# Kernel tuning notes

Hardware: AMD Instinct MI355X
Metric: run time of the kernel (lower is better)

## Reference

```python
import jax, jax.numpy as jnp
import numpy as np

N, F_T, F_P = 10000, 128, 64
MAIN_CH, SEC_CH = 7, 32


def _glorot(key, shape):
    fan_in, fan_out = shape[0], shape[1]
    lim = np.sqrt(6.0 / (fan_in + fan_out))
    return jax.random.uniform(key, shape, jnp.float32, -lim, lim)


def setup_inputs() -> dict:
    key = jax.random.key(0)
    ks = jax.random.split(key, 16)
    return {
        "temporal_features": jax.random.normal(ks[0], (N, F_T), jnp.float32),
        "A": jax.random.uniform(ks[1], (N, N), jnp.float32) / 100.0,
        "path_features": jax.random.normal(ks[2], (N, F_P), jnp.float32),
        # secondary ARMAConv: in F_T -> SEC_CH
        "Ws1": _glorot(ks[3], (F_T, SEC_CH)),
        "Ws2": _glorot(ks[4], (F_T, SEC_CH)),
        "bs": jnp.zeros((SEC_CH,), jnp.float32),
        # main2 ARMAConv: in SEC_CH+F_P -> MAIN_CH
        "Wm2a": _glorot(ks[5], (SEC_CH + F_P, MAIN_CH)),
        "Wm2b": _glorot(ks[6], (SEC_CH + F_P, MAIN_CH)),
        "bm2": jnp.zeros((MAIN_CH,), jnp.float32),
        # main ARMAConv: in F_T+F_P -> MAIN_CH
        "Wma": _glorot(ks[7], (F_T + F_P, MAIN_CH)),
        "Wmb": _glorot(ks[8], (F_T + F_P, MAIN_CH)),
        "bm": jnp.zeros((MAIN_CH,), jnp.float32),
        # scalar combine weights (v_bias_out init 1.0, v_bias_out2 init 0.0;
        # use small random values so both branches carry gradient)
        "v1": jax.random.normal(ks[9], (), jnp.float32) + 1.0,
        "v2": jax.random.normal(ks[10], (), jnp.float32),
    }


def _arma_gcs(x, A, W1, W2, b):
    # one ARMA graph-conv step (iterations=1, order=1, dropout off at eval):
    # A @ (x W1) + x W2 + b
    return A @ (x @ W1) + x @ W2 + b


def reference(temporal_features, A, path_features,
              Ws1, Ws2, bs, Wm2a, Wm2b, bm2, Wma, Wmb, bm, v1, v2):
    # secondary conv: gcn_activation=relu, activation=relu -> relu once
    sec = jax.nn.relu(_arma_gcs(temporal_features, A, Ws1, Ws2, bs))
    sec = jnp.concatenate([sec, path_features], axis=-1)          # [N, SEC+F_P]
    main_sec = _arma_gcs(sec, A, Wm2a, Wm2b, bm2)                 # [N, MAIN_CH]
    main_in = jnp.concatenate([temporal_features, path_features], axis=-1)
    main = _arma_gcs(main_in, A, Wma, Wmb, bm)                    # [N, MAIN_CH]
    # stack([v2*main, v1*main_sec], -1).mean(-1) then softmax
    combined = 0.5 * (v2 * main + v1 * main_sec)
    return jax.nn.softmax(combined, axis=-1)
```

## Files before the change

### kernel.cpp

```cpp
#include <hip/hip_runtime.h>
#include <math.h>

#define N_NODES 10000
#define FT 128
#define FP 64
#define SEC 32
#define MC 7
#define C1 39
#define KTILE 64
#define RB 64
#define NTILES 157
#define KZ 4

__global__ __launch_bounds__(256) void k1_lin(
    const float* __restrict__ T, const float* __restrict__ P,
    const float* __restrict__ Ws1, const float* __restrict__ Ws2,
    const float* __restrict__ bs, const float* __restrict__ Wma,
    const float* __restrict__ Wmb, const float* __restrict__ bm,
    float* __restrict__ P1, float* __restrict__ Z2, float* __restrict__ Zm) {
  __shared__ float Tl[8 * FT];
  __shared__ float Pl[8 * FP];
  int t = threadIdx.x;
  int r0 = blockIdx.x * 8;
  #pragma unroll
  for (int j = 0; j < 4; ++j) {
    int f = t + 256 * j;
    int r = f >> 7, k = f & 127;
    int row = r0 + r;
    Tl[f] = (row < N_NODES) ? T[row * FT + k] : 0.f;
  }
  #pragma unroll
  for (int j = 0; j < 2; ++j) {
    int f = t + 256 * j;
    int r = f >> 6, k = f & 63;
    int row = r0 + r;
    Pl[f] = (row < N_NODES) ? P[row * FP + k] : 0.f;
  }
  __syncthreads();
  int r = t >> 5, c = t & 31;
  int row = r0 + r;
  const float* trow = &Tl[r * FT];
  const float* prow = &Pl[r * FP];
  float y1 = 0.f, z2 = 0.f;
  for (int k = 0; k < FT; ++k) {
    float tv = trow[k];
    y1 += tv * Ws1[k * SEC + c];
    z2 += tv * Ws2[k * SEC + c];
  }
  z2 += bs[c];
  if (row < N_NODES) {
    P1[row * C1 + c] = y1;
    Z2[row * SEC + c] = z2;
  }
  if (c < MC) {
    float ym = 0.f, zm = 0.f;
    for (int k = 0; k < FT; ++k) {
      float tv = trow[k];
      ym += tv * Wma[k * MC + c];
      zm += tv * Wmb[k * MC + c];
    }
    for (int u = 0; u < FP; ++u) {
      float pv = prow[u];
      ym += pv * Wma[(FT + u) * MC + c];
      zm += pv * Wmb[(FT + u) * MC + c];
    }
    zm += bm[c];
    if (row < N_NODES) {
      P1[row * C1 + SEC + c] = ym;
      Zm[row * MC + c] = zm;
    }
  }
}

__global__ __launch_bounds__(256) void k2_spmm(
    const float* __restrict__ A, const float* __restrict__ P1,
    float* __restrict__ Spart) {
  __shared__ float Al[5248];
  __shared__ float Yl[KTILE * 40];
  int t = threadIdx.x;
  int r0 = blockIdx.x * RB;
  int kz = blockIdx.y;
  int w = t >> 6, r = t & 63;
  float acc[C1];
  #pragma unroll
  for (int c = 0; c < C1; ++c) acc[c] = 0.f;

  for (int tile = kz; tile < NTILES; tile += KZ) {
    int kt = tile * KTILE;
    __syncthreads();
    #pragma unroll
    for (int j = 0; j < 4; ++j) {
      int f = t + 256 * j;
      int rr = f >> 4, c4 = (f & 15) * 4;
      int row = r0 + rr, k = kt + c4;
      float4 v = make_float4(0.f, 0.f, 0.f, 0.f);
      if (row < N_NODES && k < N_NODES)
        v = *(const float4*)&A[(size_t)row * N_NODES + k];
      float* d = &Al[rr * 65 + c4];
      d[0] = v.x; d[1] = v.y; d[2] = v.z; d[3] = v.w;
    }
    #pragma unroll
    for (int j = 0; j < 10; ++j) {
      int s = t + 256 * j;
      int kk = s / 40, cc = s - kk * 40;
      int kr = kt + kk;
      float v = 0.f;
      if (cc < C1 && kr < N_NODES) v = P1[kr * C1 + cc];
      Yl[s] = v;
    }
    __syncthreads();
    for (int j = 0; j < 16; ++j) {
      int kk = 4 * j + w;
      float a = Al[r * 65 + kk];
      const float* yrow = &Yl[kk * 40];
      #pragma unroll
      for (int c = 0; c < C1; ++c) acc[c] += a * yrow[c];
    }
  }
  __syncthreads();
  if (w & 1) {
    float* dst = &Al[(w >> 1) * 2624 + r * 41];
    #pragma unroll
    for (int c = 0; c < C1; ++c) dst[c] = acc[c];
  }
  __syncthreads();
  if (!(w & 1)) {
    const float* src = &Al[(w >> 1) * 2624 + r * 41];
    #pragma unroll
    for (int c = 0; c < C1; ++c) acc[c] += src[c];
  }
  __syncthreads();
  if (w == 2) {
    float* dst = &Al[r * 41];
    #pragma unroll
    for (int c = 0; c < C1; ++c) dst[c] = acc[c];
  }
  __syncthreads();
  if (w == 0) {
    const float* src = &Al[r * 41];
    #pragma unroll
    for (int c = 0; c < C1; ++c) acc[c] += src[c];
    int row = r0 + r;
    if (row < N_NODES) {
      float* dst = &Spart[((size_t)kz * N_NODES + row) * C1];
      #pragma unroll
      for (int c = 0; c < C1; ++c) dst[c] = acc[c];
    }
  }
}

__global__ __launch_bounds__(256) void k2b(
    const float* __restrict__ Spart, const float* __restrict__ Z2,
    const float* __restrict__ Zm, const float* __restrict__ v2p,
    float* __restrict__ sec, float* __restrict__ M0) {
  int g = blockIdx.x * 256 + threadIdx.x;
  if (g >= N_NODES * C1) return;
  int row = g / C1, c = g - row * C1;
  const size_t stride = (size_t)N_NODES * C1;
  float s = Spart[g] + Spart[stride + g] + Spart[2 * stride + g] + Spart[3 * stride + g];
  if (c < SEC) {
    s += Z2[row * SEC + c];
    sec[row * SEC + c] = fmaxf(s, 0.f);
  } else {
    int j = c - SEC;
    s += Zm[row * MC + j];
    M0[row * MC + j] = 0.5f * v2p[0] * s;
  }
}

__global__ __launch_bounds__(256) void k2c(
    const float* __restrict__ sec, const float* __restrict__ P,
    const float* __restrict__ Wm2a, const float* __restrict__ Wm2b,
    const float* __restrict__ bm2, const float* __restrict__ v1p,
    const float* __restrict__ M0, float* __restrict__ Y2, float* __restrict__ C0) {
  int g = blockIdx.x * 256 + threadIdx.x;
  if (g >= N_NODES * MC) return;
  int row = g / MC, j = g - row * MC;
  float y = 0.f, z = 0.f;
  for (int c = 0; c < SEC; ++c) {
    float sv = sec[row * SEC + c];
    y += sv * Wm2a[c * MC + j];
    z += sv * Wm2b[c * MC + j];
  }
  for (int u = 0; u < FP; ++u) {
    float pv = P[row * FP + u];
    y += pv * Wm2a[(SEC + u) * MC + j];
    z += pv * Wm2b[(SEC + u) * MC + j];
  }
  z += bm2[j];
  Y2[g] = y;
  C0[g] = M0[g] + 0.5f * v1p[0] * z;
}

__global__ __launch_bounds__(256) void k3_spmm(
    const float* __restrict__ A, const float* __restrict__ Y2,
    float* __restrict__ S2part) {
  __shared__ float Al[4160];
  __shared__ float Yl[KTILE * 8];
  int t = threadIdx.x;
  int r0 = blockIdx.x * RB;
  int kz = blockIdx.y;
  int w = t >> 6, r = t & 63;
  float acc[MC];
  #pragma unroll
  for (int c = 0; c < MC; ++c) acc[c] = 0.f;

  for (int tile = kz; tile < NTILES; tile += KZ) {
    int kt = tile * KTILE;
    __syncthreads();
    #pragma unroll
    for (int j = 0; j < 4; ++j) {
      int f = t + 256 * j;
      int rr = f >> 4, c4 = (f & 15) * 4;
      int row = r0 + rr, k = kt + c4;
      float4 v = make_float4(0.f, 0.f, 0.f, 0.f);
      if (row < N_NODES && k < N_NODES)
        v = *(const float4*)&A[(size_t)row * N_NODES + k];
      float* d = &Al[rr * 65 + c4];
      d[0] = v.x; d[1] = v.y; d[2] = v.z; d[3] = v.w;
    }
    #pragma unroll
    for (int j = 0; j < 2; ++j) {
      int s = t + 256 * j;
      int kk = s >> 3, cc = s & 7;
      int kr = kt + kk;
      float v = 0.f;
      if (cc < MC && kr < N_NODES) v = Y2[kr * MC + cc];
      Yl[s] = v;
    }
    __syncthreads();
    for (int j = 0; j < 16; ++j) {
      int kk = 4 * j + w;
      float a = Al[r * 65 + kk];
      const float* yrow = &Yl[kk * 8];
      #pragma unroll
      for (int c = 0; c < MC; ++c) acc[c] += a * yrow[c];
    }
  }
  __syncthreads();
  if (w & 1) {
    float* dst = &Al[(w >> 1) * 512 + r * 8];
    #pragma unroll
    for (int c = 0; c < MC; ++c) dst[c] = acc[c];
  }
  __syncthreads();
  if (!(w & 1)) {
    const float* src = &Al[(w >> 1) * 512 + r * 8];
    #pragma unroll
    for (int c = 0; c < MC; ++c) acc[c] += src[c];
  }
  __syncthreads();
  if (w == 2) {
    float* dst = &Al[r * 8];
    #pragma unroll
    for (int c = 0; c < MC; ++c) dst[c] = acc[c];
  }
  __syncthreads();
  if (w == 0) {
    const float* src = &Al[r * 8];
    #pragma unroll
    for (int c = 0; c < MC; ++c) acc[c] += src[c];
    int row = r0 + r;
    if (row < N_NODES) {
      float* dst = &S2part[((size_t)kz * N_NODES + row) * MC];
      #pragma unroll
      for (int c = 0; c < MC; ++c) dst[c] = acc[c];
    }
  }
}

__global__ __launch_bounds__(256) void k3b(
    const float* __restrict__ S2part, const float* __restrict__ C0,
    const float* __restrict__ v1p, float* __restrict__ out) {
  int row = blockIdx.x * 256 + threadIdx.x;
  if (row >= N_NODES) return;
  float v1h = 0.5f * v1p[0];
  const size_t stride = (size_t)N_NODES * MC;
  float comb[MC];
  float mx = -1e30f;
  #pragma unroll
  for (int j = 0; j < MC; ++j) {
    int g = row * MC + j;
    float s = S2part[g] + S2part[stride + g] + S2part[2 * stride + g] + S2part[3 * stride + g];
    float cv = C0[g] + v1h * s;
    comb[j] = cv;
    mx = fmaxf(mx, cv);
  }
  float sum = 0.f;
  #pragma unroll
  for (int j = 0; j < MC; ++j) {
    comb[j] = expf(comb[j] - mx);
    sum += comb[j];
  }
  float inv = 1.f / sum;
  #pragma unroll
  for (int j = 0; j < MC; ++j) out[row * MC + j] = comb[j] * inv;
}

extern "C" void kernel_launch(void* const* d_in, const int* in_sizes, int n_in,
                              void* d_out, int out_size, void* d_ws, size_t ws_size,
                              hipStream_t stream) {
  const float* T    = (const float*)d_in[0];
  const float* A    = (const float*)d_in[1];
  const float* P    = (const float*)d_in[2];
  const float* Ws1  = (const float*)d_in[3];
  const float* Ws2  = (const float*)d_in[4];
  const float* bs   = (const float*)d_in[5];
  const float* Wm2a = (const float*)d_in[6];
  const float* Wm2b = (const float*)d_in[7];
  const float* bm2  = (const float*)d_in[8];
  const float* Wma  = (const float*)d_in[9];
  const float* Wmb  = (const float*)d_in[10];
  const float* bm   = (const float*)d_in[11];
  const float* v1   = (const float*)d_in[12];
  const float* v2   = (const float*)d_in[13];
  float* out = (float*)d_out;

  float* ws = (float*)d_ws;
  float* P1     = ws;
  float* Z2     = P1 + (size_t)N_NODES * C1;
  float* Zm     = Z2 + (size_t)N_NODES * SEC;
  float* Spart  = Zm + (size_t)N_NODES * MC;
  float* sec    = Spart + (size_t)4 * N_NODES * C1;
  float* M0     = sec + (size_t)N_NODES * SEC;
  float* Y2     = M0 + (size_t)N_NODES * MC;
  float* C0     = Y2 + (size_t)N_NODES * MC;
  float* S2part = C0 + (size_t)N_NODES * MC;

  hipLaunchKernelGGL(k1_lin, dim3((N_NODES + 7) / 8), dim3(256), 0, stream,
                     T, P, Ws1, Ws2, bs, Wma, Wmb, bm, P1, Z2, Zm);
  hipLaunchKernelGGL(k2_spmm, dim3(NTILES, KZ), dim3(256), 0, stream, A, P1, Spart);
  hipLaunchKernelGGL(k2b, dim3((N_NODES * C1 + 255) / 256), dim3(256), 0, stream,
                     Spart, Z2, Zm, v2, sec, M0);
  hipLaunchKernelGGL(k2c, dim3((N_NODES * MC + 255) / 256), dim3(256), 0, stream,
                     sec, P, Wm2a, Wm2b, bm2, v1, M0, Y2, C0);
  hipLaunchKernelGGL(k3_spmm, dim3(NTILES, KZ), dim3(256), 0, stream, A, Y2, S2part);
  hipLaunchKernelGGL(k3b, dim3((N_NODES + 255) / 256), dim3(256), 0, stream,
                     S2part, C0, v1, out);
}
```

Baseline: 944.3 us.

## Use split-bf16 MFMA for dense A products with atomic split-K reduction

Both dense A-matmuls now run on MFMA 16x16x32 bf16 instructions. A and the feature matrices are split into hi/lo bf16 pairs and multiplied as three products to keep near-fp32 accuracy. Partial sums across eight K-splits are combined with atomicAdd into a zeroed buffer, replacing the four-way partial buffers and their reduction pass. The linear kernels are restructured to process 16 rows per block and write transposed bf16 features. The kernels remain bound by streaming the 400MB A twice, and the atomics and bf16 splitting add overhead and rounding risk.

```diff
diff --git a/kernel.cpp b/kernel.cpp
--- a/kernel.cpp
+++ b/kernel.cpp
@@ -1,170 +1,188 @@
 #include <hip/hip_runtime.h>
+#include <stdint.h>
 #include <math.h>
 
 #define N_NODES 10000
-#define FT 128
-#define FP 64
-#define SEC 32
-#define MC 7
-#define C1 39
-#define KTILE 64
-#define RB 64
+#define NPAD 10048
+#define KZ 8
 #define NTILES 157
-#define KZ 4
-
-__global__ __launch_bounds__(256) void k1_lin(
+
+using short8 = __attribute__((ext_vector_type(8))) short;
+using f32x4  = __attribute__((ext_vector_type(4))) float;
+
+__device__ __forceinline__ uint32_t fbits(float x){ union{float f;uint32_t u;} v; v.f=x; return v.u; }
+__device__ __forceinline__ float    fval(uint32_t u){ union{float f;uint32_t u;} v; v.u=u; return v.f; }
+
+__device__ __forceinline__ void split1(float a, uint16_t& h, uint16_t& l){
+  uint32_t ua = fbits(a);
+  float lo = a - fval(ua & 0xFFFF0000u);
+  h = (uint16_t)(ua >> 16);
+  l = (uint16_t)(fbits(lo) >> 16);
+}
+
+__device__ __forceinline__ void split2pack(float x, float y, uint32_t& hp, uint32_t& lp){
+  uint32_t ux = fbits(x), uy = fbits(y);
+  float lx = x - fval(ux & 0xFFFF0000u);
+  float ly = y - fval(uy & 0xFFFF0000u);
+  hp = (uy & 0xFFFF0000u) | (ux >> 16);
+  lp = (fbits(ly) & 0xFFFF0000u) | (fbits(lx) >> 16);
+}
+
+__global__ __launch_bounds__(256) void k1(
     const float* __restrict__ T, const float* __restrict__ P,
     const float* __restrict__ Ws1, const float* __restrict__ Ws2,
     const float* __restrict__ bs, const float* __restrict__ Wma,
     const float* __restrict__ Wmb, const float* __restrict__ bm,
-    float* __restrict__ P1, float* __restrict__ Z2, float* __restrict__ Zm) {
-  __shared__ float Tl[8 * FT];
-  __shared__ float Pl[8 * FP];
+    uint16_t* __restrict__ Yth, uint16_t* __restrict__ Ytl,
+    float* __restrict__ Z2, float* __restrict__ Zm) {
+  __shared__ float Xl[16 * 192];
+  __shared__ float RedY[16 * 7], RedZ[16 * 7];
   int t = threadIdx.x;
-  int r0 = blockIdx.x * 8;
-  #pragma unroll
-  for (int j = 0; j < 4; ++j) {
-    int f = t + 256 * j;
-    int r = f >> 7, k = f & 127;
+  int r0 = blockIdx.x * 16;
+  for (int s = t; s < 768; s += 256) {
+    int r = s / 48, c4 = (s % 48) * 4;
+    const float* src = (c4 < 128) ? &T[(size_t)(r0 + r) * 128 + c4]
+                                  : &P[(size_t)(r0 + r) * 64 + (c4 - 128)];
+    *(float4*)&Xl[r * 192 + c4] = *(const float4*)src;
+  }
+  __syncthreads();
+  {
+    int c = t & 31, r = t >> 5;
+    float y0 = 0, z0 = 0, y1 = 0, z1 = 0;
+    const float* x0 = &Xl[r * 192];
+    const float* x1 = &Xl[(r + 8) * 192];
+    #pragma unroll 8
+    for (int k = 0; k < 128; ++k) {
+      float w1 = Ws1[k * 32 + c], w2 = Ws2[k * 32 + c];
+      float a0 = x0[k], a1 = x1[k];
+      y0 += a0 * w1; z0 += a0 * w2;
+      y1 += a1 * w1; z1 += a1 * w2;
+    }
+    int rowA = r0 + r, rowB = r0 + r + 8;
+    float bsv = bs[c];
+    Z2[rowA * 32 + c] = z0 + bsv;
+    Z2[rowB * 32 + c] = z1 + bsv;
+    uint16_t h, l;
+    split1(y0, h, l); Yth[c * NPAD + rowA] = h; Ytl[c * NPAD + rowA] = l;
+    split1(y1, h, l); Yth[c * NPAD + rowB] = h; Ytl[c * NPAD + rowB] = l;
+  }
+  int u = t & 15, r = t >> 4;
+  int j = u % 7, half = u / 7;
+  float ym = 0, zm = 0;
+  if (u < 14) {
+    int kb = half * 96;
+    const float* xr = &Xl[r * 192];
+    #pragma unroll 4
+    for (int i = 0; i < 96; ++i) {
+      int k = kb + i;
+      float wa = Wma[k * 7 + j], wb = Wmb[k * 7 + j];
+      float xv = xr[k];
+      ym += xv * wa; zm += xv * wb;
+    }
+    if (half == 1) { RedY[r * 7 + j] = ym; RedZ[r * 7 + j] = zm; }
+  }
+  __syncthreads();
+  if (u < 7) {
+    ym += RedY[r * 7 + j]; zm += RedZ[r * 7 + j];
     int row = r0 + r;
-    Tl[f] = (row < N_NODES) ? T[row * FT + k] : 0.f;
-  }
-  #pragma unroll
-  for (int j = 0; j < 2; ++j) {
-    int f = t + 256 * j;
-    int r = f >> 6, k = f & 63;
-    int row = r0 + r;
-    Pl[f] = (row < N_NODES) ? P[row * FP + k] : 0.f;
-  }
-  __syncthreads();
-  int r = t >> 5, c = t & 31;
-  int row = r0 + r;
-  const float* trow = &Tl[r * FT];
-  const float* prow = &Pl[r * FP];
-  float y1 = 0.f, z2 = 0.f;
-  for (int k = 0; k < FT; ++k) {
-    float tv = trow[k];
-    y1 += tv * Ws1[k * SEC + c];
-    z2 += tv * Ws2[k * SEC + c];
-  }
-  z2 += bs[c];
-  if (row < N_NODES) {
-    P1[row * C1 + c] = y1;
-    Z2[row * SEC + c] = z2;
-  }
-  if (c < MC) {
-    float ym = 0.f, zm = 0.f;
-    for (int k = 0; k < FT; ++k) {
-      float tv = trow[k];
-      ym += tv * Wma[k * MC + c];
-      zm += tv * Wmb[k * MC + c];
-    }
-    for (int u = 0; u < FP; ++u) {
-      float pv = prow[u];
-      ym += pv * Wma[(FT + u) * MC + c];
-      zm += pv * Wmb[(FT + u) * MC + c];
-    }
-    zm += bm[c];
-    if (row < N_NODES) {
-      P1[row * C1 + SEC + c] = ym;
-      Zm[row * MC + c] = zm;
-    }
-  }
-}
-
-__global__ __launch_bounds__(256) void k2_spmm(
-    const float* __restrict__ A, const float* __restrict__ P1,
-    float* __restrict__ Spart) {
-  __shared__ float Al[5248];
-  __shared__ float Yl[KTILE * 40];
+    uint16_t h, l;
+    split1(ym, h, l);
+    Yth[(32 + j) * NPAD + row] = h; Ytl[(32 + j) * NPAD + row] = l;
+    Zm[row * 7 + j] = zm + bm[j];
+  }
+}
+
+template<int NCF, int NC, int CST>
+__global__ __launch_bounds__(256) void k_spmm(
+    const float* __restrict__ A, const uint16_t* __restrict__ Yth,
+    const uint16_t* __restrict__ Ytl, float* __restrict__ Sacc) {
+  __shared__ uint16_t Ah[64 * 72];
+  __shared__ uint16_t Al[64 * 72];
+  __shared__ uint16_t Yh[NCF * 16 * 72];
+  __shared__ uint16_t Yl[NCF * 16 * 72];
   int t = threadIdx.x;
-  int r0 = blockIdx.x * RB;
+  int r0 = blockIdx.x * 64;
   int kz = blockIdx.y;
-  int w = t >> 6, r = t & 63;
-  float acc[C1];
-  #pragma unroll
-  for (int c = 0; c < C1; ++c) acc[c] = 0.f;
+  int w = t >> 6, lane = t & 63;
+  int m = lane & 15, q = lane >> 4;
+  f32x4 acc[NCF];
+  #pragma unroll
+  for (int f = 0; f < NCF; ++f) acc[f] = (f32x4){0.f, 0.f, 0.f, 0.f};
 
   for (int tile = kz; tile < NTILES; tile += KZ) {
-    int kt = tile * KTILE;
+    int kt = tile * 64;
     __syncthreads();
     #pragma unroll
-    for (int j = 0; j < 4; ++j) {
-      int f = t + 256 * j;
-      int rr = f >> 4, c4 = (f & 15) * 4;
+    for (int jj = 0; jj < 4; ++jj) {
+      int fi = t + 256 * jj;
+      int rr = fi >> 4, c4 = (fi & 15) * 4;
       int row = r0 + rr, k = kt + c4;
       float4 v = make_float4(0.f, 0.f, 0.f, 0.f);
       if (row < N_NODES && k < N_NODES)
         v = *(const float4*)&A[(size_t)row * N_NODES + k];
-      float* d = &Al[rr * 65 + c4];
-      d[0] = v.x; d[1] = v.y; d[2] = v.z; d[3] = v.w;
-    }
+      uint32_t h0, l0, h1, l1;
+      split2pack(v.x, v.y, h0, l0);
+      split2pack(v.z, v.w, h1, l1);
+      uint2 hh; hh.x = h0; hh.y = h1;
+      uint2 ll; ll.x = l0; ll.y = l1;
+      *(uint2*)&Ah[rr * 72 + c4] = hh;
+      *(uint2*)&Al[rr * 72 + c4] = ll;
+    }
+    for (int s = t; s < NCF * 16 * 32; s += 256) {
+      int c = s >> 5, kk = s & 31;
+      int k2i = kt + 2 * kk;
+      uint32_t vh = 0, vl = 0;
+      if (c < NC && k2i < N_NODES) {
+        vh = *(const uint32_t*)&Yth[(size_t)c * NPAD + k2i];
+        vl = *(const uint32_t*)&Ytl[(size_t)c * NPAD + k2i];
+      }
+      *(uint32_t*)&Yh[c * 72 + 2 * kk] = vh;
+      *(uint32_t*)&Yl[c * 72 + 2 * kk] = vl;
+    }
+    __syncthreads();
     #pragma unroll
-    for (int j = 0; j < 10; ++j) {
-      int s = t + 256 * j;
-      int kk = s / 40, cc = s - kk * 40;
-      int kr = kt + kk;
-      float v = 0.f;
-      if (cc < C1 && kr < N_NODES) v = P1[kr * C1 + cc];
-      Yl[s] = v;
-    }
-    __syncthreads();
-    for (int j = 0; j < 16; ++j) {
-      int kk = 4 * j + w;
-      float a = Al[r * 65 + kk];
-      const float* yrow = &Yl[kk * 40];
+    for (int ks = 0; ks < 2; ++ks) {
+      int ko = ks * 32 + q * 8;
+      short8 ah = *(const short8*)&Ah[(16 * w + m) * 72 + ko];
+      short8 al = *(const short8*)&Al[(16 * w + m) * 72 + ko];
       #pragma unroll
-      for (int c = 0; c < C1; ++c) acc[c] += a * yrow[c];
-    }
-  }
-  __syncthreads();
-  if (w & 1) {
-    float* dst = &Al[(w >> 1) * 2624 + r * 41];
-    #pragma unroll
-    for (int c = 0; c < C1; ++c) dst[c] = acc[c];
-  }
-  __syncthreads();
-  if (!(w & 1)) {
-    const float* src = &Al[(w >> 1) * 2624 + r * 41];
-    #pragma unroll
-    for (int c = 0; c < C1; ++c) acc[c] += src[c];
-  }
-  __syncthreads();
-  if (w == 2) {
-    float* dst = &Al[r * 41];
-    #pragma unroll
-    for (int c = 0; c < C1; ++c) dst[c] = acc[c];
-  }
-  __syncthreads();
-  if (w == 0) {
-    const float* src = &Al[r * 41];
-    #pragma unroll
-    for (int c = 0; c < C1; ++c) acc[c] += src[c];
-    int row = r0 + r;
-    if (row < N_NODES) {
-      float* dst = &Spart[((size_t)kz * N_NODES + row) * C1];
+      for (int f = 0; f < NCF; ++f) {
+        short8 yh = *(const short8*)&Yh[(16 * f + m) * 72 + ko];
+        short8 yl = *(const short8*)&Yl[(16 * f + m) * 72 + ko];
+        acc[f] = __builtin_amdgcn_mfma_f32_16x16x32_bf16(ah, yh, acc[f], 0, 0, 0);
+        acc[f] = __builtin_amdgcn_mfma_f32_16x16x32_bf16(ah, yl, acc[f], 0, 0, 0);
+        acc[f] = __builtin_amdgcn_mfma_f32_16x16x32_bf16(al, yh, acc[f], 0, 0, 0);
+      }
+    }
+  }
+  int rb = r0 + 16 * w + q * 4;
+  #pragma unroll
+  for (int f = 0; f < NCF; ++f) {
+    int col = 16 * f + m;
+    if (col < CST) {
       #pragma unroll
-      for (int c = 0; c < C1; ++c) dst[c] = acc[c];
+      for (int r4 = 0; r4 < 4; ++r4) {
+        int row = rb + r4;
+        if (row < N_NODES) atomicAdd(&Sacc[(size_t)row * CST + col], acc[f][r4]);
+      }
     }
   }
 }
 
 __global__ __launch_bounds__(256) void k2b(
-    const float* __restrict__ Spart, const float* __restrict__ Z2,
+    const float* __restrict__ Sacc, const float* __restrict__ Z2,
     const float* __restrict__ Zm, const float* __restrict__ v2p,
     float* __restrict__ sec, float* __restrict__ M0) {
   int g = blockIdx.x * 256 + threadIdx.x;
-  if (g >= N_NODES * C1) return;
-  int row = g / C1, c = g - row * C1;
-  const size_t stride = (size_t)N_NODES * C1;
-  float s = Spart[g] + Spart[stride + g] + Spart[2 * stride + g] + Spart[3 * stride + g];
-  if (c < SEC) {
-    s += Z2[row * SEC + c];
-    sec[row * SEC + c] = fmaxf(s, 0.f);
-  } else {
-    int j = c - SEC;
-    s += Zm[row * MC + j];
-    M0[row * MC + j] = 0.5f * v2p[0] * s;
+  if (g >= N_NODES * 40) return;
+  int row = g / 40, c = g % 40;
+  if (c < 32) {
+    float s = Sacc[g] + Z2[row * 32 + c];
+    sec[row * 32 + c] = fmaxf(s, 0.f);
+  } else if (c < 39) {
+    int j = c - 32;
+    float s = Sacc[g] + Zm[row * 7 + j];
+    M0[row * 7 + j] = 0.5f * v2p[0] * s;
   }
 }
 
@@ -172,129 +190,64 @@
     const float* __restrict__ sec, const float* __restrict__ P,
     const float* __restrict__ Wm2a, const float* __restrict__ Wm2b,
     const float* __restrict__ bm2, const float* __restrict__ v1p,
-    const float* __restrict__ M0, float* __restrict__ Y2, float* __restrict__ C0) {
-  int g = blockIdx.x * 256 + threadIdx.x;
-  if (g >= N_NODES * MC) return;
-  int row = g / MC, j = g - row * MC;
-  float y = 0.f, z = 0.f;
-  for (int c = 0; c < SEC; ++c) {
-    float sv = sec[row * SEC + c];
-    y += sv * Wm2a[c * MC + j];
-    z += sv * Wm2b[c * MC + j];
-  }
-  for (int u = 0; u < FP; ++u) {
-    float pv = P[row * FP + u];
-    y += pv * Wm2a[(SEC + u) * MC + j];
-    z += pv * Wm2b[(SEC + u) * MC + j];
-  }
-  z += bm2[j];
-  Y2[g] = y;
-  C0[g] = M0[g] + 0.5f * v1p[0] * z;
-}
-
-__global__ __launch_bounds__(256) void k3_spmm(
-    const float* __restrict__ A, const float* __restrict__ Y2,
-    float* __restrict__ S2part) {
-  __shared__ float Al[4160];
-  __shared__ float Yl[KTILE * 8];
+    const float* __restrict__ M0,
+    uint16_t* __restrict__ Y2th, uint16_t* __restrict__ Y2tl,
+    float* __restrict__ C0) {
+  __shared__ float Xc[16 * 96];
+  __shared__ float RedY[16 * 7], RedZ[16 * 7];
   int t = threadIdx.x;
-  int r0 = blockIdx.x * RB;
-  int kz = blockIdx.y;
-  int w = t >> 6, r = t & 63;
-  float acc[MC];
-  #pragma unroll
-  for (int c = 0; c < MC; ++c) acc[c] = 0.f;
-
-  for (int tile = kz; tile < NTILES; tile += KZ) {
-    int kt = tile * KTILE;
-    __syncthreads();
-    #pragma unroll
-    for (int j = 0; j < 4; ++j) {
-      int f = t + 256 * j;
-      int rr = f >> 4, c4 = (f & 15) * 4;
-      int row = r0 + rr, k = kt + c4;
-      float4 v = make_float4(0.f, 0.f, 0.f, 0.f);
-      if (row < N_NODES && k < N_NODES)
-        v = *(const float4*)&A[(size_t)row * N_NODES + k];
-      float* d = &Al[rr * 65 + c4];
-      d[0] = v.x; d[1] = v.y; d[2] = v.z; d[3] = v.w;
-    }
-    #pragma unroll
-    for (int j = 0; j < 2; ++j) {
-      int s = t + 256 * j;
-      int kk = s >> 3, cc = s & 7;
-      int kr = kt + kk;
-      float v = 0.f;
-      if (cc < MC && kr < N_NODES) v = Y2[kr * MC + cc];
-      Yl[s] = v;
-    }
-    __syncthreads();
-    for (int j = 0; j < 16; ++j) {
-      int kk = 4 * j + w;
-      float a = Al[r * 65 + kk];
-      const float* yrow = &Yl[kk * 8];
-      #pragma unroll
-      for (int c = 0; c < MC; ++c) acc[c] += a * yrow[c];
-    }
-  }
-  __syncthreads();
-  if (w & 1) {
-    float* dst = &Al[(w >> 1) * 512 + r * 8];
-    #pragma unroll
-    for (int c = 0; c < MC; ++c) dst[c] = acc[c];
-  }
-  __syncthreads();
-  if (!(w & 1)) {
-    const float* src = &Al[(w >> 1) * 512 + r * 8];
-    #pragma unroll
-    for (int c = 0; c < MC; ++c) acc[c] += src[c];
-  }
-  __syncthreads();
-  if (w == 2) {
-    float* dst = &Al[r * 8];
-    #pragma unroll
-    for (int c = 0; c < MC; ++c) dst[c] = acc[c];
-  }
-  __syncthreads();
-  if (w == 0) {
-    const float* src = &Al[r * 8];
-    #pragma unroll
-    for (int c = 0; c < MC; ++c) acc[c] += src[c];
+  int r0 = blockIdx.x * 16;
+  for (int s = t; s < 384; s += 256) {
+    int r = s / 24, c4 = (s % 24) * 4;
+    const float* src = (c4 < 32) ? &sec[(size_t)(r0 + r) * 32 + c4]
+                                 : &P[(size_t)(r0 + r) * 64 + (c4 - 32)];
+    *(float4*)&Xc[r * 96 + c4] = *(const float4*)src;
+  }
+  __syncthreads();
+  int u = t & 15, r = t >> 4;
+  int j = u % 7, half = u / 7;
+  float y = 0, z = 0;
+  if (u < 14) {
+    int kb = half * 48;
+    const float* xr = &Xc[r * 96];
+    #pragma unroll 4
+    for (int i = 0; i < 48; ++i) {
+      int k = kb + i;
+      y += xr[k] * Wm2a[k * 7 + j];
+      z += xr[k] * Wm2b[k * 7 + j];
+    }
+    if (half == 1) { RedY[r * 7 + j] = y; RedZ[r * 7 + j] = z; }
+  }
+  __syncthreads();
+  if (u < 7) {
+    y += RedY[r * 7 + j]; z += RedZ[r * 7 + j];
     int row = r0 + r;
-    if (row < N_NODES) {
-      float* dst = &S2part[((size_t)kz * N_NODES + row) * MC];
-      #pragma unroll
-      for (int c = 0; c < MC; ++c) dst[c] = acc[c];
-    }
+    uint16_t h, l;
+    split1(y, h, l);
+    Y2th[j * NPAD + row] = h; Y2tl[j * NPAD + row] = l;
+    C0[row * 7 + j] = M0[row * 7 + j] + 0.5f * v1p[0] * (z + bm2[j]);
   }
 }
 
 __global__ __launch_bounds__(256) void k3b(
-    const float* __restrict__ S2part, const float* __restrict__ C0,
+    const float* __restrict__ S2, const float* __restrict__ C0,
     const float* __restrict__ v1p, float* __restrict__ out) {
   int row = blockIdx.x * 256 + threadIdx.x;
   if (row >= N_NODES) return;
   float v1h = 0.5f * v1p[0];
-  const size_t stride = (size_t)N_NODES * MC;
-  float comb[MC];
+  float comb[7];
   float mx = -1e30f;
   #pragma unroll
-  for (int j = 0; j < MC; ++j) {
-    int g = row * MC + j;
-    float s = S2part[g] + S2part[stride + g] + S2part[2 * stride + g] + S2part[3 * stride + g];
-    float cv = C0[g] + v1h * s;
-    comb[j] = cv;
-    mx = fmaxf(mx, cv);
+  for (int j = 0; j < 7; ++j) {
+    float cv = C0[row * 7 + j] + v1h * S2[row * 8 + j];
+    comb[j] = cv; mx = fmaxf(mx, cv);
   }
   float sum = 0.f;
   #pragma unroll
-  for (int j = 0; j < MC; ++j) {
-    comb[j] = expf(comb[j] - mx);
-    sum += comb[j];
-  }
+  for (int j = 0; j < 7; ++j) { comb[j] = expf(comb[j] - mx); sum += comb[j]; }
   float inv = 1.f / sum;
   #pragma unroll
-  for (int j = 0; j < MC; ++j) out[row * MC + j] = comb[j] * inv;
+  for (int j = 0; j < 7; ++j) out[row * 7 + j] = comb[j] * inv;
 }
 
 extern "C" void kernel_launch(void* const* d_in, const int* in_sizes, int n_in,
@@ -317,24 +270,30 @@
   float* out = (float*)d_out;
 
   float* ws = (float*)d_ws;
-  float* P1     = ws;
-  float* Z2     = P1 + (size_t)N_NODES * C1;
-  float* Zm     = Z2 + (size_t)N_NODES * SEC;
-  float* Spart  = Zm + (size_t)N_NODES * MC;
-  float* sec    = Spart + (size_t)4 * N_NODES * C1;
-  float* M0     = sec + (size_t)N_NODES * SEC;
-  float* Y2     = M0 + (size_t)N_NODES * MC;
-  float* C0     = Y2 + (size_t)N_NODES * MC;
-  float* S2part = C0 + (size_t)N_NODES * MC;
-
-  hipLaunchKernelGGL(k1_lin, dim3((N_NODES + 7) / 8), dim3(256), 0, stream,
-                     T, P, Ws1, Ws2, bs, Wma, Wmb, bm, P1, Z2, Zm);
-  hipLaunchKernelGGL(k2_spmm, dim3(NTILES, KZ), dim3(256), 0, stream, A, P1, Spart);
-  hipLaunchKernelGGL(k2b, dim3((N_NODES * C1 + 255) / 256), dim3(256), 0, stream,
-                     Spart, Z2, Zm, v2, sec, M0);
-  hipLaunchKernelGGL(k2c, dim3((N_NODES * MC + 255) / 256), dim3(256), 0, stream,
-                     sec, P, Wm2a, Wm2b, bm2, v1, M0, Y2, C0);
-  hipLaunchKernelGGL(k3_spmm, dim3(NTILES, KZ), dim3(256), 0, stream, A, Y2, S2part);
+  float* Sacc = ws;
+  float* S2   = Sacc + 400000;
+  float* Z2   = S2 + 80000;
+  float* Zm   = Z2 + 320000;
+  float* sec  = Zm + 70000;
+  float* M0   = sec + 320000;
+  float* C0   = M0 + 70000;
+  uint16_t* Yth  = (uint16_t*)(C0 + 70000);
+  uint16_t* Ytl  = Yth + 40 * NPAD;
+  uint16_t* Y2th = Ytl + 40 * NPAD;
+  uint16_t* Y2tl = Y2th + 8 * NPAD;
+
+  hipMemsetAsync(Sacc, 0, (size_t)(400000 + 80000) * sizeof(float), stream);
+
+  hipLaunchKernelGGL(k1, dim3(625), dim3(256), 0, stream,
+                     T, P, Ws1, Ws2, bs, Wma, Wmb, bm, Yth, Ytl, Z2, Zm);
+  hipLaunchKernelGGL((k_spmm<3, 39, 40>), dim3(NTILES, KZ), dim3(256), 0, stream,
+                     A, Yth, Ytl, Sacc);
+  hipLaunchKernelGGL(k2b, dim3((N_NODES * 40 + 255) / 256), dim3(256), 0, stream,
+                     Sacc, Z2, Zm, v2, sec, M0);
+  hipLaunchKernelGGL(k2c, dim3(625), dim3(256), 0, stream,
+                     sec, P, Wm2a, Wm2b, bm2, v1, M0, Y2th, Y2tl, C0);
+  hipLaunchKernelGGL((k_spmm<1, 7, 8>), dim3(NTILES, KZ), dim3(256), 0, stream,
+                     A, Y2th, Y2tl, S2);
   hipLaunchKernelGGL(k3b, dim3((N_NODES + 255) / 256), dim3(256), 0, stream,
-                     S2part, C0, v1, out);
-}
+                     S2, C0, v1, out);
+}
```

Result: faster. 792.2 us (-16.1%).
